# Performance work log

Measured on AMD Instinct MI355X. Metric: run time of the kernel, lower is better.

Reference implementation:

```python
import jax, jax.numpy as jnp
import numpy as np

B, L, D, H = 4, 2048, 2048, 16
HEAD_DIM = D // H
EPS = 1e-5


def rmsnorm(x, w):
    # fp32 RMSNorm as in the torch module
    xf = x.astype(jnp.float32)
    rms = jnp.sqrt(jnp.mean(xf * xf, axis=-1, keepdims=True) + EPS)
    return xf / rms * w


def apply_rope(x, freqs):
    # x: (..., D) with interleaved even/odd pairs; freqs: (2, L, D/2) = (sin, cos)
    sin, cos = freqs[0], freqs[1]
    xr = x.reshape(*x.shape[:-1], D // 2, 2)
    x_even, x_odd = xr[..., 0], xr[..., 1]
    e = x_even * cos - x_odd * sin
    o = x_odd * cos + x_even * sin
    return jnp.stack([e, o], axis=-1).reshape(x.shape)


def setup_inputs() -> dict:
    key = jax.random.key(0)
    k0, k1, k2 = jax.random.split(key, 3)
    x_BLD = jax.random.normal(k0, (B, L, D), dtype=jnp.float32)
    # realistic RoPE angle table over the full dim (matches module usage)
    t = jnp.arange(L, dtype=jnp.float32)[:, None]
    inv_freq = 1.0 / (10000.0 ** (jnp.arange(D // 2, dtype=jnp.float32) / (D // 2)))
    ang = t * inv_freq[None, :]                      # (L, D/2)
    freqs = jnp.stack([jnp.sin(ang), jnp.cos(ang)])  # (2, L, D/2)
    wqkv = jax.random.normal(k1, (3 * D, D), dtype=jnp.float32) * 0.02
    wo = jax.random.normal(k2, (D, D), dtype=jnp.float32) * 0.02
    q_norm_w = jnp.ones((D,), dtype=jnp.float32)
    k_norm_w = jnp.ones((D,), dtype=jnp.float32)
    return {"x_BLD": x_BLD, "freqs": freqs, "wqkv": wqkv, "wo": wo,
            "q_norm_w": q_norm_w, "k_norm_w": k_norm_w}


def reference(x_BLD, freqs, wqkv, wo, q_norm_w, k_norm_w):
    dtype = x_BLD.dtype
    qkv = x_BLD @ wqkv.T                             # (B, L, 3D)
    q, k, v = jnp.split(qkv, 3, axis=-1)
    q = apply_rope(rmsnorm(q, q_norm_w), freqs).astype(dtype)
    k = apply_rope(rmsnorm(k, k_norm_w), freqs).astype(dtype)
    # (B, L, D) -> (B, H, L, hd)
    q = q.reshape(B, L, H, HEAD_DIM).transpose(0, 2, 1, 3)
    k = k.reshape(B, L, H, HEAD_DIM).transpose(0, 2, 1, 3)
    v = v.reshape(B, L, H, HEAD_DIM).transpose(0, 2, 1, 3)
    scale = HEAD_DIM ** -0.5
    scores = jnp.einsum('bhqd,bhkd->bhqk', q, k) * scale
    attn = jax.nn.softmax(scores, axis=-1)
    out = jnp.einsum('bhqk,bhkd->bhqd', attn, v)
    out = out.transpose(0, 2, 1, 3).reshape(B, L, D)
    return out @ wo.T
```

## Files before the change

kernel.cpp:

```cpp
#include <hip/hip_runtime.h>
#include <stdint.h>
#include <stddef.h>

typedef unsigned short u16;
typedef __bf16 bf16x8 __attribute__((ext_vector_type(8)));
typedef float  f32x4  __attribute__((ext_vector_type(4)));
typedef float  f32x16 __attribute__((ext_vector_type(16)));

__device__ __forceinline__ float bf2f(u16 u){ return __uint_as_float(((unsigned)u)<<16); }
__device__ __forceinline__ u16 f2bf(float f){
  unsigned u = __float_as_uint(f);
  return (u16)((u + 0x7fffu + ((u>>16)&1u)) >> 16);
}
__device__ __forceinline__ void gl_lds16(const void* g, void* s){
  __builtin_amdgcn_global_load_lds(
      (__attribute__((address_space(1))) void*)(void*)g,
      (__attribute__((address_space(3))) void*)s, 16, 0, 0);
}

__global__ void k_f2bf(const float* __restrict__ in, u16* __restrict__ out, int n4){
  int i = blockIdx.x*256 + threadIdx.x;
  if (i < n4){
    float4 v = ((const float4*)in)[i];
    ((ushort4*)out)[i] = make_ushort4(f2bf(v.x), f2bf(v.y), f2bf(v.z), f2bf(v.w));
  }
}

template<int BF16OUT>
__global__ __launch_bounds__(256,2) void k_gemm_bt(const u16* __restrict__ A,
                                                   const u16* __restrict__ Bm,
                                                   void* __restrict__ Cout,
                                                   int M, int N, int K){
  __shared__ __align__(16) u16 As[128*64];
  __shared__ __align__(16) u16 Bs[128*64];
  const int tid = threadIdx.x, w = tid>>6, ln = tid&63;
  const int l16 = ln&15, quad = ln>>4;
  const int wm = w&1, wn = w>>1;
  const int m0 = blockIdx.y*128, n0 = blockIdx.x*128;
  const f32x4 z4 = {0.f,0.f,0.f,0.f};
  f32x4 acc[4][4];
  #pragma unroll
  for (int i=0;i<4;++i)
    #pragma unroll
    for (int j=0;j<4;++j) acc[i][j] = z4;

  const int nkb = K >> 6;
  for (int kb=0; kb<nkb; ++kb){
    __syncthreads();
    const int ka = kb*64;
    #pragma unroll
    for (int j=0;j<4;++j){
      gl_lds16(A  + (size_t)(m0 + w*32 + j*8 + (ln>>3))*K + ka + (ln&7)*8,
               &As[(w*32+j*8)*64]);
      gl_lds16(Bm + (size_t)(n0 + w*32 + j*8 + (ln>>3))*K + ka + (ln&7)*8,
               &Bs[(w*32+j*8)*64]);
    }
    __builtin_amdgcn_s_waitcnt(0);
    __syncthreads();
    #pragma unroll
    for (int k0=0;k0<64;k0+=32){
      bf16x8 a[4], b[4];
      #pragma unroll
      for (int mt=0;mt<4;++mt) a[mt] = *(const bf16x8*)&As[(wm*64+mt*16+l16)*64 + k0 + quad*8];
      #pragma unroll
      for (int nt=0;nt<4;++nt) b[nt] = *(const bf16x8*)&Bs[(wn*64+nt*16+l16)*64 + k0 + quad*8];
      #pragma unroll
      for (int mt=0;mt<4;++mt)
        #pragma unroll
        for (int nt=0;nt<4;++nt)
          acc[mt][nt] = __builtin_amdgcn_mfma_f32_16x16x32_bf16(a[mt], b[nt], acc[mt][nt], 0,0,0);
    }
  }
  #pragma unroll
  for (int mt=0;mt<4;++mt)
    #pragma unroll
    for (int nt=0;nt<4;++nt)
      #pragma unroll
      for (int j=0;j<4;++j){
        int row = m0 + wm*64 + mt*16 + quad*4 + j;
        int col = n0 + wn*64 + nt*16 + l16;
        if (BF16OUT) ((u16*)Cout)[(size_t)row*N + col] = f2bf(acc[mt][nt][j]);
        else         ((float*)Cout)[(size_t)row*N + col] = acc[mt][nt][j];
      }
}

__global__ void k_prep_qk(const u16* __restrict__ qkv, const float* __restrict__ freqs,
                          const float* __restrict__ qw, const float* __restrict__ kw,
                          u16* __restrict__ Qo, u16* __restrict__ Ko){
  const int row = blockIdx.x;
  const int b = row >> 11, l = row & 2047;
  const int tid = threadIdx.x;
  const u16* qr = qkv + (size_t)row*6144;
  float qe[4], qo[4], ke[4], ko_[4];
  float sq = 0.f, sk = 0.f;
  #pragma unroll
  for (int it=0; it<4; ++it){
    int p = tid + it*256;
    ushort2 q2 = ((const ushort2*)qr)[p];
    ushort2 k2 = ((const ushort2*)(qr+2048))[p];
    qe[it]=bf2f(q2.x); qo[it]=bf2f(q2.y);
    ke[it]=bf2f(k2.x); ko_[it]=bf2f(k2.y);
    sq += qe[it]*qe[it] + qo[it]*qo[it];
    sk += ke[it]*ke[it] + ko_[it]*ko_[it];
  }
  #pragma unroll
  for (int off=32; off; off>>=1){ sq += __shfl_xor(sq, off); sk += __shfl_xor(sk, off); }
  __shared__ float red[8];
  if ((tid&63)==0){ red[tid>>6]=sq; red[4+(tid>>6)]=sk; }
  __syncthreads();
  sq = red[0]+red[1]+red[2]+red[3];
  sk = red[4]+red[5]+red[6]+red[7];
  const float rq = rsqrtf(sq*(1.f/2048.f) + 1e-5f);
  const float rk = rsqrtf(sk*(1.f/2048.f) + 1e-5f);
  const float QS = 0.08838834764831845f * 1.4426950408889634f;
  #pragma unroll
  for (int it=0; it<4; ++it){
    int p = tid + it*256;
    float sn = freqs[(size_t)l*1024 + p];
    float cs = freqs[2097152 + (size_t)l*1024 + p];
    float2 w2q = ((const float2*)qw)[p];
    float2 w2k = ((const float2*)kw)[p];
    int h = p>>6, dd2 = p&63;
    size_t o = ((size_t)(b*16+h)*2048 + l)*64 + dd2;
    float a = qe[it]*rq*w2q.x, c = qo[it]*rq*w2q.y;
    ((ushort2*)Qo)[o] = make_ushort2(f2bf((a*cs - c*sn)*QS), f2bf((c*cs + a*sn)*QS));
    a = ke[it]*rk*w2k.x; c = ko_[it]*rk*w2k.y;
    ((ushort2*)Ko)[o] = make_ushort2(f2bf(a*cs - c*sn), f2bf(c*cs + a*sn));
  }
}

__global__ void k_prep_v(const u16* __restrict__ qkv, u16* __restrict__ Vt){
  const int lt = blockIdx.x, bh = blockIdx.y;
  const int b = bh>>4, h = bh&15;
  __shared__ u16 tile[64][136];
  const int tid = threadIdx.x;
  #pragma unroll
  for (int it=0; it<32; ++it){
    int idx = it*256 + tid;
    int lo = idx >> 7, dd = idx & 127;
    tile[lo][dd] = qkv[(size_t)(b*2048 + lt*64 + lo)*6144 + 4096 + h*128 + dd];
  }
  __syncthreads();
  #pragma unroll
  for (int it=0; it<32; ++it){
    int idx = it*256 + tid;
    int dd = idx >> 6, lo = idx & 63;
    Vt[((size_t)bh*128 + dd)*2048 + lt*64 + lo] = tile[lo][dd];
  }
}

__global__ __launch_bounds__(256,2) void k_flash(const u16* __restrict__ Q,
                                                 const u16* __restrict__ Kg,
                                                 const u16* __restrict__ Vt,
                                                 u16* __restrict__ O){
  __shared__ __align__(16) u16 KV[128*136];
  __shared__ __align__(16) u16 Pt[4][32*136];
  const int qt = blockIdx.x, bh = blockIdx.y;
  const int tid = threadIdx.x, w = tid>>6, ln = tid&63;
  const int l31 = ln&31, hi = ln>>5;
  const int b = bh>>4, h = bh&15;
  const size_t qkbase = (size_t)bh*(2048*128);

  const int srow = tid>>4, scol = tid&15;
  const u16* kgp = Kg + qkbase + (size_t)srow*128 + scol*8;
  const u16* vgp = Vt + (size_t)bh*(128*2048) + (size_t)srow*2048 + scol*8;
  u16* ldsw = &KV[srow*136 + scol*8];

  bf16x8 qf[8];
  {
    const u16* qp = Q + qkbase + (size_t)(qt*128 + w*32 + l31)*128 + hi*8;
    #pragma unroll
    for (int kk=0; kk<8; ++kk) qf[kk] = *(const bf16x8*)(qp + kk*16);
  }

  f32x16 o[4];
  #pragma unroll
  for (int dt=0; dt<4; ++dt)
    #pragma unroll
    for (int r=0; r<16; ++r) o[dt][r] = 0.f;
  float m_ = -1e30f, l_ = 0.f;

  bf16x8 kreg[8], vreg[8];
  #pragma unroll
  for (int it=0; it<8; ++it) kreg[it] = *(const bf16x8*)(kgp + (size_t)it*16*128);

  u16* Pw = &Pt[w][0];

  for (int kt=0; kt<16; ++kt){
    __syncthreads();
    #pragma unroll
    for (int it=0; it<8; ++it) *(bf16x8*)(ldsw + it*16*136) = kreg[it];
    #pragma unroll
    for (int it=0; it<8; ++it)
      vreg[it] = *(const bf16x8*)(vgp + kt*128 + (size_t)it*16*2048);
    __syncthreads();
    f32x16 s[4];
    #pragma unroll
    for (int t=0;t<4;++t)
      #pragma unroll
      for (int r=0;r<16;++r) s[t][r] = 0.f;
    #pragma unroll
    for (int kk=0; kk<8; ++kk){
      #pragma unroll
      for (int t=0; t<4; ++t){
        bf16x8 a = *(const bf16x8*)&KV[(t*32 + l31)*136 + kk*16 + hi*8];
        s[t] = __builtin_amdgcn_mfma_f32_32x32x16_bf16(a, qf[kk], s[t], 0,0,0);
      }
    }
    float mc = -1e30f;
    #pragma unroll
    for (int t=0;t<4;++t)
      #pragma unroll
      for (int r=0;r<16;++r) mc = fmaxf(mc, s[t][r]);
    mc = fmaxf(mc, __shfl_xor(mc, 32));
    const float mn = fmaxf(m_, mc);
    const float al = exp2f(m_ - mn);
    m_ = mn;
    float rs = 0.f;
    #pragma unroll
    for (int t=0;t<4;++t)
      #pragma unroll
      for (int r=0;r<16;++r){ float p = exp2f(s[t][r] - mn); rs += p; s[t][r] = p; }
    rs += __shfl_xor(rs, 32);
    l_ = l_*al + rs;
    #pragma unroll
    for (int t=0;t<4;++t)
      #pragma unroll
      for (int g=0;g<4;++g)
        *(ushort4*)&Pw[l31*136 + t*32 + g*8 + hi*4] =
          make_ushort4(f2bf(s[t][g*4+0]), f2bf(s[t][g*4+1]),
                       f2bf(s[t][g*4+2]), f2bf(s[t][g*4+3]));
    #pragma unroll
    for (int dt=0;dt<4;++dt)
      #pragma unroll
      for (int r=0;r<16;++r) o[dt][r] *= al;
    __syncthreads();
    #pragma unroll
    for (int it=0; it<8; ++it) *(bf16x8*)(ldsw + it*16*136) = vreg[it];
    if (kt < 15){
      #pragma unroll
      for (int it=0; it<8; ++it)
        kreg[it] = *(const bf16x8*)(kgp + (size_t)(kt+1)*128*128 + (size_t)it*16*128);
    }
    __syncthreads();
    #pragma unroll
    for (int kk=0; kk<8; ++kk){
      bf16x8 bp = *(const bf16x8*)&Pw[l31*136 + kk*16 + hi*8];
      #pragma unroll
      for (int dt=0; dt<4; ++dt){
        bf16x8 a = *(const bf16x8*)&KV[(dt*32 + l31)*136 + kk*16 + hi*8];
        o[dt] = __builtin_amdgcn_mfma_f32_32x32x16_bf16(a, bp, o[dt], 0,0,0);
      }
    }
  }
  const float inv = 1.f/l_;
  __syncthreads();
  #pragma unroll
  for (int dt=0;dt<4;++dt)
    #pragma unroll
    for (int g=0;g<4;++g)
      *(ushort4*)&KV[(w*32+l31)*136 + dt*32 + g*8 + hi*4] =
        make_ushort4(f2bf(o[dt][g*4+0]*inv), f2bf(o[dt][g*4+1]*inv),
                     f2bf(o[dt][g*4+2]*inv), f2bf(o[dt][g*4+3]*inv));
  __syncthreads();
  #pragma unroll
  for (int it=0; it<8; ++it){
    int q = it*16 + srow;
    bf16x8 vv = *(const bf16x8*)&KV[q*136 + scol*8];
    *(bf16x8*)&O[(size_t)(b*2048 + qt*128 + q)*2048 + h*128 + scol*8] = vv;
  }
}

extern "C" void kernel_launch(void* const* d_in, const int* in_sizes, int n_in,
                              void* d_out, int out_size, void* d_ws, size_t ws_size,
                              hipStream_t stream){
  const float* x     = (const float*)d_in[0];
  const float* freqs = (const float*)d_in[1];
  const float* wqkv  = (const float*)d_in[2];
  const float* wo    = (const float*)d_in[3];
  const float* qw    = (const float*)d_in[4];
  const float* kw    = (const float*)d_in[5];
  char* ws = (char*)d_ws;
  u16* xbf    = (u16*)(ws);
  u16* wqkvbf = (u16*)(ws + 33554432);
  u16* wobf   = (u16*)(ws + 58720256);
  u16* qkvbf  = (u16*)(ws + 67108864);
  u16* Qbf    = (u16*)(ws + 167772160);
  u16* Kbf    = (u16*)(ws + 201326592);
  u16* Vtbf   = (u16*)(ws + 234881024);
  u16* Abf    = qkvbf;
  float* out  = (float*)d_out;

  k_f2bf<<<16384,256,0,stream>>>(x,    xbf,    4194304);
  k_f2bf<<<12288,256,0,stream>>>(wqkv, wqkvbf, 3145728);
  k_f2bf<<< 4096,256,0,stream>>>(wo,   wobf,   1048576);
  k_gemm_bt<1><<<dim3(48,64),256,0,stream>>>(xbf, wqkvbf, qkvbf, 8192, 6144, 2048);
  k_prep_qk<<<8192,256,0,stream>>>(qkvbf, freqs, qw, kw, Qbf, Kbf);
  k_prep_v<<<dim3(32,64),256,0,stream>>>(qkvbf, Vtbf);
  k_flash<<<dim3(16,64),256,0,stream>>>(Qbf, Kbf, Vtbf, Abf);
  k_gemm_bt<0><<<dim3(16,64),256,0,stream>>>(Abf, wobf, out, 8192, 2048, 2048);
}
```

Measured before the change: 734.9 us.

## Keep P in registers via lane shuffles and split K/V LDS buffers

The flash attention kernel stops staging the softmax probabilities P through per-wave LDS. It now packs them into bf16 MFMA B-operand fragments in registers, using cross-half-wave shuffles. K and V get separate LDS buffers and are both prefetched for the next tile right after the single barrier, which removes two of the four block-wide barriers per iteration. This raises register pressure from holding kreg, vreg and bfrag together under launch_bounds(256,2), so spilling or lower occupancy is a risk.

```diff
diff --git a/kernel.cpp b/kernel.cpp
--- a/kernel.cpp
+++ b/kernel.cpp
@@ -153,8 +153,8 @@
                                                  const u16* __restrict__ Kg,
                                                  const u16* __restrict__ Vt,
                                                  u16* __restrict__ O){
-  __shared__ __align__(16) u16 KV[128*136];
-  __shared__ __align__(16) u16 Pt[4][32*136];
+  __shared__ __align__(16) u16 Kt[128*136];
+  __shared__ __align__(16) u16 Vs[128*136];
   const int qt = blockIdx.x, bh = blockIdx.y;
   const int tid = threadIdx.x, w = tid>>6, ln = tid&63;
   const int l31 = ln&31, hi = ln>>5;
@@ -164,7 +164,8 @@
   const int srow = tid>>4, scol = tid&15;
   const u16* kgp = Kg + qkbase + (size_t)srow*128 + scol*8;
   const u16* vgp = Vt + (size_t)bh*(128*2048) + (size_t)srow*2048 + scol*8;
-  u16* ldsw = &KV[srow*136 + scol*8];
+  u16* kld = &Kt[srow*136 + scol*8];
+  u16* vld = &Vs[srow*136 + scol*8];
 
   bf16x8 qf[8];
   {
@@ -183,17 +184,26 @@
   bf16x8 kreg[8], vreg[8];
   #pragma unroll
   for (int it=0; it<8; ++it) kreg[it] = *(const bf16x8*)(kgp + (size_t)it*16*128);
-
-  u16* Pw = &Pt[w][0];
+  #pragma unroll
+  for (int it=0; it<8; ++it) vreg[it] = *(const bf16x8*)(vgp + (size_t)it*16*2048);
+
+  union U4 { unsigned u[4]; bf16x8 v; };
 
   for (int kt=0; kt<16; ++kt){
     __syncthreads();
     #pragma unroll
-    for (int it=0; it<8; ++it) *(bf16x8*)(ldsw + it*16*136) = kreg[it];
-    #pragma unroll
-    for (int it=0; it<8; ++it)
-      vreg[it] = *(const bf16x8*)(vgp + kt*128 + (size_t)it*16*2048);
+    for (int it=0; it<8; ++it) *(bf16x8*)(kld + it*16*136) = kreg[it];
+    #pragma unroll
+    for (int it=0; it<8; ++it) *(bf16x8*)(vld + it*16*136) = vreg[it];
     __syncthreads();
+    if (kt < 15){
+      #pragma unroll
+      for (int it=0; it<8; ++it)
+        kreg[it] = *(const bf16x8*)(kgp + (size_t)(kt+1)*128*128 + (size_t)it*16*128);
+      #pragma unroll
+      for (int it=0; it<8; ++it)
+        vreg[it] = *(const bf16x8*)(vgp + (kt+1)*128 + (size_t)it*16*2048);
+    }
     f32x16 s[4];
     #pragma unroll
     for (int t=0;t<4;++t)
@@ -203,7 +213,7 @@
     for (int kk=0; kk<8; ++kk){
       #pragma unroll
       for (int t=0; t<4; ++t){
-        bf16x8 a = *(const bf16x8*)&KV[(t*32 + l31)*136 + kk*16 + hi*8];
+        bf16x8 a = *(const bf16x8*)&Kt[(t*32 + l31)*136 + kk*16 + hi*8];
         s[t] = __builtin_amdgcn_mfma_f32_32x32x16_bf16(a, qf[kk], s[t], 0,0,0);
       }
     }
@@ -217,39 +227,48 @@
     const float al = exp2f(m_ - mn);
     m_ = mn;
     float rs = 0.f;
-    #pragma unroll
-    for (int t=0;t<4;++t)
-      #pragma unroll
-      for (int r=0;r<16;++r){ float p = exp2f(s[t][r] - mn); rs += p; s[t][r] = p; }
+    bf16x8 bfrag[8];
+    #pragma unroll
+    for (int t=0;t<4;++t){
+      unsigned pk[4][2];
+      #pragma unroll
+      for (int g=0;g<4;++g){
+        float p0 = exp2f(s[t][g*4+0] - mn);
+        float p1 = exp2f(s[t][g*4+1] - mn);
+        float p2 = exp2f(s[t][g*4+2] - mn);
+        float p3 = exp2f(s[t][g*4+3] - mn);
+        rs += (p0+p1)+(p2+p3);
+        pk[g][0] = (unsigned)f2bf(p0) | ((unsigned)f2bf(p1)<<16);
+        pk[g][1] = (unsigned)f2bf(p2) | ((unsigned)f2bf(p3)<<16);
+      }
+      unsigned a0 = (unsigned)__shfl_xor((int)(hi ? pk[0][0] : pk[1][0]), 32);
+      unsigned a1 = (unsigned)__shfl_xor((int)(hi ? pk[0][1] : pk[1][1]), 32);
+      unsigned b0 = (unsigned)__shfl_xor((int)(hi ? pk[2][0] : pk[3][0]), 32);
+      unsigned b1 = (unsigned)__shfl_xor((int)(hi ? pk[2][1] : pk[3][1]), 32);
+      U4 u0, u1;
+      u0.u[0] = hi ? a0       : pk[0][0];
+      u0.u[1] = hi ? a1       : pk[0][1];
+      u0.u[2] = hi ? pk[1][0] : a0;
+      u0.u[3] = hi ? pk[1][1] : a1;
+      u1.u[0] = hi ? b0       : pk[2][0];
+      u1.u[1] = hi ? b1       : pk[2][1];
+      u1.u[2] = hi ? pk[3][0] : b0;
+      u1.u[3] = hi ? pk[3][1] : b1;
+      bfrag[t*2+0] = u0.v;
+      bfrag[t*2+1] = u1.v;
+    }
     rs += __shfl_xor(rs, 32);
     l_ = l_*al + rs;
     #pragma unroll
-    for (int t=0;t<4;++t)
-      #pragma unroll
-      for (int g=0;g<4;++g)
-        *(ushort4*)&Pw[l31*136 + t*32 + g*8 + hi*4] =
-          make_ushort4(f2bf(s[t][g*4+0]), f2bf(s[t][g*4+1]),
-                       f2bf(s[t][g*4+2]), f2bf(s[t][g*4+3]));
-    #pragma unroll
     for (int dt=0;dt<4;++dt)
       #pragma unroll
       for (int r=0;r<16;++r) o[dt][r] *= al;
-    __syncthreads();
-    #pragma unroll
-    for (int it=0; it<8; ++it) *(bf16x8*)(ldsw + it*16*136) = vreg[it];
-    if (kt < 15){
-      #pragma unroll
-      for (int it=0; it<8; ++it)
-        kreg[it] = *(const bf16x8*)(kgp + (size_t)(kt+1)*128*128 + (size_t)it*16*128);
-    }
-    __syncthreads();
     #pragma unroll
     for (int kk=0; kk<8; ++kk){
-      bf16x8 bp = *(const bf16x8*)&Pw[l31*136 + kk*16 + hi*8];
       #pragma unroll
       for (int dt=0; dt<4; ++dt){
-        bf16x8 a = *(const bf16x8*)&KV[(dt*32 + l31)*136 + kk*16 + hi*8];
-        o[dt] = __builtin_amdgcn_mfma_f32_32x32x16_bf16(a, bp, o[dt], 0,0,0);
+        bf16x8 a = *(const bf16x8*)&Vs[(dt*32 + l31)*136 + kk*16 + hi*8];
+        o[dt] = __builtin_amdgcn_mfma_f32_32x32x16_bf16(a, bfrag[kk], o[dt], 0,0,0);
       }
     }
   }
@@ -259,14 +278,14 @@
   for (int dt=0;dt<4;++dt)
     #pragma unroll
     for (int g=0;g<4;++g)
-      *(ushort4*)&KV[(w*32+l31)*136 + dt*32 + g*8 + hi*4] =
+      *(ushort4*)&Kt[(w*32+l31)*136 + dt*32 + g*8 + hi*4] =
         make_ushort4(f2bf(o[dt][g*4+0]*inv), f2bf(o[dt][g*4+1]*inv),
                      f2bf(o[dt][g*4+2]*inv), f2bf(o[dt][g*4+3]*inv));
   __syncthreads();
   #pragma unroll
   for (int it=0; it<8; ++it){
     int q = it*16 + srow;
-    bf16x8 vv = *(const bf16x8*)&KV[q*136 + scol*8];
+    bf16x8 vv = *(const bf16x8*)&Kt[q*136 + scol*8];
     *(bf16x8*)&O[(size_t)(b*2048 + qt*128 + q)*2048 + h*128 + scol*8] = vv;
   }
 }
```

Measured after the change: 738.1 us. No clear change (+0.4%).
